# Optimization experiments

Hardware: AMD Instinct MI355X
Metric: run time of the kernel (lower is better)

The kernel has to match this reference:

```python
import jax, jax.numpy as jnp
import numpy as np

MAX_SIZE = 650   # hard-coded node count in the original module
HIDDEN = 512     # hidden_dim
BATCH = 512      # batch_size (conv4 out channels)
IN_DIM = 512
N_EDGES = 150000


def _segment_softmax(e, dst, n):
    # torch_geometric.utils.softmax over destination-node segments
    m = jax.ops.segment_max(e, dst, num_segments=n)
    ex = jnp.exp(e - m[dst])
    s = jax.ops.segment_sum(ex, dst, num_segments=n)
    return ex / (s[dst] + 1e-16)


def _gat_conv(x, src, dst, W, a_src, a_dst, b, n, neg_slope=0.2):
    # PyG GATConv, heads=1, edge_dim=None (edge_attr ignored)
    h = x @ W                            # [n, out]
    al_s = h @ a_src                     # [n] per-node source attention logit
    al_d = h @ a_dst                     # [n] per-node dest attention logit
    e = jax.nn.leaky_relu(al_s[src] + al_d[dst], neg_slope)   # [E]
    alpha = _segment_softmax(e, dst, n)                        # [E]
    out = jax.ops.segment_sum(alpha[:, None] * h[src], dst, num_segments=n)
    return out + b


def setup_inputs() -> dict:
    key = jax.random.key(0)
    ks = jax.random.split(key, 12)
    inp = {
        "x_s": jax.random.normal(ks[0], (400, IN_DIM), jnp.float32),
        "x_t": jax.random.normal(ks[1], (250, IN_DIM), jnp.float32),
        "edge_index": jax.random.randint(ks[2], (2, N_EDGES), 0, MAX_SIZE, dtype=jnp.int32),
        "distances": jax.random.uniform(ks[3], (N_EDGES,), jnp.float32),
        "batch": jnp.zeros((MAX_SIZE,), jnp.int32),
        "W1": jax.random.normal(ks[4], (IN_DIM, HIDDEN), jnp.float32) / np.sqrt(IN_DIM).astype(np.float32),
        "a_src1": jax.random.normal(ks[5], (HIDDEN,), jnp.float32) * 0.1,
        "a_dst1": jax.random.normal(ks[6], (HIDDEN,), jnp.float32) * 0.1,
        "b1": jnp.zeros((HIDDEN,), jnp.float32),
        "W4": jax.random.normal(ks[7], (HIDDEN, BATCH), jnp.float32) / np.sqrt(HIDDEN).astype(np.float32),
        "a_src4": jax.random.normal(ks[8], (BATCH,), jnp.float32) * 0.1,
        "a_dst4": jax.random.normal(ks[9], (BATCH,), jnp.float32) * 0.1,
        "b4": jnp.zeros((BATCH,), jnp.float32),
        "fc_w": jax.random.normal(ks[10], (1, MAX_SIZE), jnp.float32) / np.sqrt(MAX_SIZE).astype(np.float32),
        "fc_b": jnp.zeros((1,), jnp.float32),
    }
    return inp


def reference(x_s, x_t, edge_index, distances, batch,
              W1, a_src1, a_dst1, b1, W4, a_src4, a_dst4, b4, fc_w, fc_b):
    # distances (edge_attr) and batch are unpacked but unused, as in the
    # original (GATConv with edge_dim=None ignores edge_attr).
    x = jnp.concatenate([x_s, x_t], axis=0)
    pad_n = max(MAX_SIZE - x.shape[0], 0)
    x = jnp.pad(x, ((0, pad_n), (0, 0)))            # [650, IN_DIM]
    # add_self_loops=True (PyG GATConv default)
    loop = jnp.arange(MAX_SIZE, dtype=edge_index.dtype)
    src = jnp.concatenate([edge_index[0], loop])
    dst = jnp.concatenate([edge_index[1], loop])
    x = _gat_conv(x, src, dst, W1, a_src1, a_dst1, b1, MAX_SIZE)
    x = jax.nn.relu(x)
    x = _gat_conv(x, src, dst, W4, a_src4, a_dst4, b4, MAX_SIZE)
    x = jax.nn.leaky_relu(x, 0.01)                  # [650, BATCH]
    x = x.reshape(BATCH, MAX_SIZE)                  # torch .view semantics (no transpose)
    x = x @ fc_w.T + fc_b                           # [BATCH, 1]
    x = x.squeeze()[None, :]                        # [1, BATCH]
    return jax.nn.sigmoid(x)
```

## Files before the change

### kernel.cpp

```cpp
#include <hip/hip_runtime.h>
#include <math.h>

#define N_NODES 650
#define DIM     512
#define E_RAW   150000
#define E_TOT   150650

#define BM 16
#define BN 64
#define BK 32
#define KC 128
#define NZ (DIM / KC)
#define CH 1024
#define NB 64

__global__ __launch_bounds__(256)
void gemm_hp(const float* __restrict__ A, const float* __restrict__ Axt,
             const float* __restrict__ B, float* __restrict__ P,
             int M, int a_mode) {
    __shared__ float Ast[BK][BM + 2];
    __shared__ float Bs[BK][BN];
    int t  = threadIdx.x;
    int tx = t & 15, ty = t >> 4;
    int row0 = blockIdx.y * BM, col0 = blockIdx.x * BN;
    int kbase = blockIdx.z * KC;
    float acc[4] = {};

    for (int kb = kbase; kb < kbase + KC; kb += BK) {
        if (t < 128) {
            int m  = t >> 3;
            int kq = (t & 7) * 4;
            int gr = row0 + m;
            float4 v = make_float4(0.f, 0.f, 0.f, 0.f);
            if (gr < M) {
                const float* rowp;
                if (a_mode == 1)
                    rowp = (gr < 400) ? (A + (size_t)gr * DIM) : (Axt + (size_t)(gr - 400) * DIM);
                else
                    rowp = A + (size_t)gr * DIM;
                v = *(const float4*)(rowp + kb + kq);
            }
            Ast[kq + 0][m] = v.x;
            Ast[kq + 1][m] = v.y;
            Ast[kq + 2][m] = v.z;
            Ast[kq + 3][m] = v.w;
        }
        {
            int n4 = (t & 15) * 4;
            int kk = t >> 4;
            #pragma unroll
            for (int p = 0; p < 2; p++)
                *(float4*)&Bs[kk + p * 16][n4] =
                    *(const float4*)&B[(size_t)(kb + kk + p * 16) * DIM + col0 + n4];
        }
        __syncthreads();
        #pragma unroll
        for (int kk = 0; kk < BK; kk++) {
            float a = Ast[kk][ty];
            float4 b4 = *(const float4*)&Bs[kk][tx * 4];
            acc[0] += a * b4.x; acc[1] += a * b4.y;
            acc[2] += a * b4.z; acc[3] += a * b4.w;
        }
        __syncthreads();
    }

    float* Cout = P + (size_t)blockIdx.z * N_NODES * DIM;
    int gr = row0 + ty;
    if (gr < M)
        *(float4*)&Cout[(size_t)gr * DIM + col0 + tx * 4] =
            make_float4(acc[0], acc[1], acc[2], acc[3]);
}

__global__ __launch_bounds__(256)
void reduce_logits(const float* __restrict__ P,
                   const float* __restrict__ asrc, const float* __restrict__ adst,
                   float* __restrict__ h, float* __restrict__ als, float* __restrict__ ald) {
    __shared__ float red[8];
    const size_t S = (size_t)N_NODES * DIM;
    int r = blockIdx.x, t = threadIdx.x;
    size_t base = (size_t)r * DIM;
    float v0 = 0.f, v1 = 0.f;
    #pragma unroll
    for (int z = 0; z < NZ; z++) {
        v0 += P[z * S + base + t];
        v1 += P[z * S + base + t + 256];
    }
    h[base + t]       = v0;
    h[base + t + 256] = v1;
    float ps = v0 * asrc[t] + v1 * asrc[t + 256];
    float pd = v0 * adst[t] + v1 * adst[t + 256];
    #pragma unroll
    for (int o = 32; o > 0; o >>= 1) {
        ps += __shfl_down(ps, o);
        pd += __shfl_down(pd, o);
    }
    if ((t & 63) == 0) { red[t >> 6] = ps; red[4 + (t >> 6)] = pd; }
    __syncthreads();
    if (t == 0) als[r] = red[0] + red[1] + red[2] + red[3];
    if (t == 1) ald[r] = red[4] + red[5] + red[6] + red[7];
}

__global__ __launch_bounds__(256)
void count_kernel(const int* __restrict__ ei, int* __restrict__ cntb) {
    __shared__ int h[N_NODES];
    for (int l = threadIdx.x; l < N_NODES; l += 256) h[l] = 0;
    __syncthreads();
    int per = (E_TOT + NB - 1) / NB;
    int e0 = blockIdx.x * per;
    int e1 = min(e0 + per, E_TOT);
    for (int i = e0 + threadIdx.x; i < e1; i += 256) {
        int d = (i < E_RAW) ? ei[E_RAW + i] : i - E_RAW;
        atomicAdd(&h[d], 1);
    }
    __syncthreads();
    for (int l = threadIdx.x; l < N_NODES; l += 256)
        cntb[blockIdx.x * N_NODES + l] = h[l];
}

__global__ __launch_bounds__(1024)
void scanbase_kernel(const int* __restrict__ cntb, int* __restrict__ rowptr,
                     int* __restrict__ baseb) {
    __shared__ int buf[1024];
    int t = threadIdx.x;
    int tot = 0;
    if (t < N_NODES)
        for (int b = 0; b < NB; b++) tot += cntb[b * N_NODES + t];
    buf[t] = (t < N_NODES) ? tot : 0;
    __syncthreads();
    #pragma unroll
    for (int o = 1; o < 1024; o <<= 1) {
        int v = (t >= o) ? buf[t - o] : 0;
        __syncthreads();
        buf[t] += v;
        __syncthreads();
    }
    if (t < N_NODES) {
        int run = buf[t] - tot;
        rowptr[t] = run;
        for (int b = 0; b < NB; b++) {
            baseb[b * N_NODES + t] = run;
            run += cntb[b * N_NODES + t];
        }
    }
    if (t == 0) rowptr[N_NODES] = E_TOT;
}

__global__ __launch_bounds__(256)
void scatter2_kernel(const int* __restrict__ ei, const int* __restrict__ baseb,
                     int* __restrict__ ssrc) {
    __shared__ int lcur[N_NODES];
    for (int l = threadIdx.x; l < N_NODES; l += 256)
        lcur[l] = baseb[blockIdx.x * N_NODES + l];
    __syncthreads();
    int per = (E_TOT + NB - 1) / NB;
    int e0 = blockIdx.x * per;
    int e1 = min(e0 + per, E_TOT);
    for (int i = e0 + threadIdx.x; i < e1; i += 256) {
        int s, d;
        if (i < E_RAW) { s = ei[i]; d = ei[E_RAW + i]; }
        else           { s = d = i - E_RAW; }
        int pos = atomicAdd(&lcur[d], 1);
        ssrc[pos] = s;
    }
}

__global__ __launch_bounds__(256)
void spmm_kernel(const int* __restrict__ rowptr, const int* __restrict__ ssrc,
                 const float* __restrict__ als, const float* __restrict__ ald,
                 const float* __restrict__ h, const float* __restrict__ bias,
                 float slope, float* __restrict__ outm) {
    __shared__ int   sS[CH];
    __shared__ float sE[CH];
    __shared__ float red[4];
    int d = blockIdx.x;
    int t = threadIdx.x;
    int c = blockIdx.y * 256 + t;
    int r0 = rowptr[d], r1 = rowptr[d + 1];
    int deg = r1 - r0;
    float aldd = ald[d];
    float acc = 0.f, psum = 0.f;

    for (int cb = 0; cb < deg; cb += CH) {
        int n = min(CH, deg - cb);
        __syncthreads();
        for (int l = t; l < n; l += 256) {
            int s = ssrc[r0 + cb + l];
            float v = als[s] + aldd;
            v = v > 0.f ? v : 0.2f * v;
            float ex = __expf(v);
            sS[l] = s;
            sE[l] = ex;
            psum += ex;
        }
        __syncthreads();
        int e = 0;
        for (; e + 4 <= n; e += 4) {
            int   s0 = sS[e],   s1 = sS[e+1], s2 = sS[e+2], s3 = sS[e+3];
            float e0 = sE[e],   e1 = sE[e+1], e2 = sE[e+2], e3 = sE[e+3];
            float x0 = h[(size_t)s0 * DIM + c];
            float x1 = h[(size_t)s1 * DIM + c];
            float x2 = h[(size_t)s2 * DIM + c];
            float x3 = h[(size_t)s3 * DIM + c];
            acc += e0 * x0 + e1 * x1 + e2 * x2 + e3 * x3;
        }
        for (; e < n; e++)
            acc += sE[e] * h[(size_t)sS[e] * DIM + c];
    }

    #pragma unroll
    for (int o = 32; o > 0; o >>= 1) psum += __shfl_down(psum, o);
    if ((t & 63) == 0) red[t >> 6] = psum;
    __syncthreads();
    float sum = red[0] + red[1] + red[2] + red[3];
    float v = acc / (sum + 1e-16f) + bias[c];
    v = v > 0.f ? v : slope * v;
    outm[(size_t)d * DIM + c] = v;
}

__global__ void final_kernel(const float* __restrict__ o2,
                             const float* __restrict__ fcw,
                             const float* __restrict__ fcb,
                             float* __restrict__ out) {
    int b = blockIdx.x * 4 + (threadIdx.x >> 6);
    int lane = threadIdx.x & 63;
    if (b >= 512) return;
    float s = 0.f;
    for (int i = lane; i < N_NODES; i += 64)
        s += o2[b * N_NODES + i] * fcw[i];
    #pragma unroll
    for (int o = 32; o > 0; o >>= 1) s += __shfl_down(s, o);
    if (lane == 0) out[b] = 1.f / (1.f + expf(-(s + fcb[0])));
}

extern "C" void kernel_launch(void* const* d_in, const int* in_sizes, int n_in,
                              void* d_out, int out_size, void* d_ws, size_t ws_size,
                              hipStream_t stream) {
    const float* x_s   = (const float*)d_in[0];
    const float* x_t   = (const float*)d_in[1];
    const int*   ei    = (const int*)d_in[2];
    const float* W1    = (const float*)d_in[5];
    const float* asrc1 = (const float*)d_in[6];
    const float* adst1 = (const float*)d_in[7];
    const float* b1    = (const float*)d_in[8];
    const float* W4    = (const float*)d_in[9];
    const float* asrc4 = (const float*)d_in[10];
    const float* adst4 = (const float*)d_in[11];
    const float* b4    = (const float*)d_in[12];
    const float* fcw   = (const float*)d_in[13];
    const float* fcb   = (const float*)d_in[14];
    float* out = (float*)d_out;

    const size_t H_ELEMS = (size_t)N_NODES * DIM;
    float* ws = (float*)d_ws;
    int*   cntb   = (int*)ws;
    int*   baseb  = cntb + NB * N_NODES;
    int*   rowptr = baseb + NB * N_NODES;
    int*   ssrc   = rowptr + N_NODES + 1;
    float* als1   = (float*)(ssrc + E_TOT);
    float* ald1   = als1 + N_NODES;
    float* als2   = ald1 + N_NODES;
    float* ald2   = als2 + N_NODES;
    float* P      = ald2 + N_NODES;
    float* h1     = P + (size_t)NZ * H_ELEMS;
    float* o1     = h1 + H_ELEMS;
    float* h2     = h1;
    float* o2     = o1;

    dim3 gG(DIM / BN, (N_NODES + BM - 1) / BM, NZ);
    dim3 gS(N_NODES, 2);

    count_kernel<<<NB, 256, 0, stream>>>(ei, cntb);
    scanbase_kernel<<<1, 1024, 0, stream>>>(cntb, rowptr, baseb);
    scatter2_kernel<<<NB, 256, 0, stream>>>(ei, baseb, ssrc);

    gemm_hp<<<gG, 256, 0, stream>>>(x_s, x_t, W1, P, N_NODES, 1);
    reduce_logits<<<N_NODES, 256, 0, stream>>>(P, asrc1, adst1, h1, als1, ald1);
    spmm_kernel<<<gS, 256, 0, stream>>>(rowptr, ssrc, als1, ald1, h1, b1, 0.0f, o1);

    gemm_hp<<<gG, 256, 0, stream>>>(o1, nullptr, W4, P, N_NODES, 0);
    reduce_logits<<<N_NODES, 256, 0, stream>>>(P, asrc4, adst4, h2, als2, ald2);
    spmm_kernel<<<gS, 256, 0, stream>>>(rowptr, ssrc, als2, ald2, h2, b4, 0.01f, o2);

    final_kernel<<<128, 256, 0, stream>>>(o2, fcw, fcb, out);
}
```

Measured before the change: 189.1 us.

## Replace edge-gather SpMM with dense attention matrix GEMM and fuse epilogues

Each destination row's softmax weights are accumulated into a dense 650x650 attention matrix (alpha_build, using shared-memory atomics). Aggregation then runs as a dense GEMM with h, replacing the per-edge gather SpMM over about 150k edges. The GEMM tile grows to 64x64 with a 4x4 register micro-tile and split-K of 2. Bias plus ReLU for layer 1 is fused into the next GEMM's A-load, and bias plus leaky-ReLU for layer 2 into the final kernel. This trades irregular gather traffic for roughly 650^2*512 dense FLOPs per layer and extra workspace.

```diff
diff --git a/kernel.cpp b/kernel.cpp
--- a/kernel.cpp
+++ b/kernel.cpp
@@ -5,70 +5,96 @@
 #define DIM     512
 #define E_RAW   150000
 #define E_TOT   150650
-
-#define BM 16
-#define BN 64
-#define BK 32
-#define KC 128
-#define NZ (DIM / KC)
-#define CH 1024
-#define NB 64
-
-__global__ __launch_bounds__(256)
-void gemm_hp(const float* __restrict__ A, const float* __restrict__ Axt,
-             const float* __restrict__ B, float* __restrict__ P,
-             int M, int a_mode) {
-    __shared__ float Ast[BK][BM + 2];
-    __shared__ float Bs[BK][BN];
+#define NB      64
+#define A_LD    704
+#define S_H     (N_NODES * DIM)
+
+__global__ __launch_bounds__(256)
+void gemm4(const float* __restrict__ A0, const float* __restrict__ A1p,
+           const float* __restrict__ abias, const float* __restrict__ B,
+           float* __restrict__ P, int M, int lda, int Kb, int KC, int a_mode) {
+    __shared__ float Ast[32][68];
+    __shared__ float Bs[32][64];
     int t  = threadIdx.x;
     int tx = t & 15, ty = t >> 4;
-    int row0 = blockIdx.y * BM, col0 = blockIdx.x * BN;
+    int row0 = blockIdx.y * 64, col0 = blockIdx.x * 64;
     int kbase = blockIdx.z * KC;
-    float acc[4] = {};
-
-    for (int kb = kbase; kb < kbase + KC; kb += BK) {
-        if (t < 128) {
-            int m  = t >> 3;
-            int kq = (t & 7) * 4;
-            int gr = row0 + m;
-            float4 v = make_float4(0.f, 0.f, 0.f, 0.f);
-            if (gr < M) {
-                const float* rowp;
-                if (a_mode == 1)
-                    rowp = (gr < 400) ? (A + (size_t)gr * DIM) : (Axt + (size_t)(gr - 400) * DIM);
-                else
-                    rowp = A + (size_t)gr * DIM;
-                v = *(const float4*)(rowp + kb + kq);
+    float acc[4][4] = {};
+    int m   = t >> 2;
+    int kq  = (t & 3) * 4;
+    int bkk = t >> 4;
+    int bn4 = (t & 15) * 4;
+
+    for (int kb = kbase; kb < kbase + KC; kb += 32) {
+        float4 va = make_float4(0.f, 0.f, 0.f, 0.f);
+        float4 vb = make_float4(0.f, 0.f, 0.f, 0.f);
+        int gr = row0 + m;
+        if (gr < M) {
+            if (a_mode == 1) {
+                const float* rp = (gr < 400) ? (A0 + (size_t)gr * 512)
+                                             : (A1p + (size_t)(gr - 400) * 512);
+                va = *(const float4*)(rp + kb + kq);
+                vb = *(const float4*)(rp + kb + kq + 16);
+            } else if (a_mode == 2) {
+                size_t base = (size_t)gr * 512 + kb + kq;
+                float4 p0 = *(const float4*)(A0 + base);
+                float4 p1 = *(const float4*)(A1p + base);
+                float4 bb = *(const float4*)(abias + kb + kq);
+                va.x = p0.x + p1.x + bb.x; va.y = p0.y + p1.y + bb.y;
+                va.z = p0.z + p1.z + bb.z; va.w = p0.w + p1.w + bb.w;
+                p0 = *(const float4*)(A0 + base + 16);
+                p1 = *(const float4*)(A1p + base + 16);
+                bb = *(const float4*)(abias + kb + kq + 16);
+                vb.x = p0.x + p1.x + bb.x; vb.y = p0.y + p1.y + bb.y;
+                vb.z = p0.z + p1.z + bb.z; vb.w = p0.w + p1.w + bb.w;
+                va.x = fmaxf(va.x, 0.f); va.y = fmaxf(va.y, 0.f);
+                va.z = fmaxf(va.z, 0.f); va.w = fmaxf(va.w, 0.f);
+                vb.x = fmaxf(vb.x, 0.f); vb.y = fmaxf(vb.y, 0.f);
+                vb.z = fmaxf(vb.z, 0.f); vb.w = fmaxf(vb.w, 0.f);
+            } else {
+                const float* rp = A0 + (size_t)gr * lda;
+                va = *(const float4*)(rp + kb + kq);
+                vb = *(const float4*)(rp + kb + kq + 16);
             }
-            Ast[kq + 0][m] = v.x;
-            Ast[kq + 1][m] = v.y;
-            Ast[kq + 2][m] = v.z;
-            Ast[kq + 3][m] = v.w;
-        }
+        }
+        Ast[kq + 0][m] = va.x; Ast[kq + 1][m] = va.y;
+        Ast[kq + 2][m] = va.z; Ast[kq + 3][m] = va.w;
+        Ast[kq + 16][m] = vb.x; Ast[kq + 17][m] = vb.y;
+        Ast[kq + 18][m] = vb.z; Ast[kq + 19][m] = vb.w;
         {
-            int n4 = (t & 15) * 4;
-            int kk = t >> 4;
-            #pragma unroll
-            for (int p = 0; p < 2; p++)
-                *(float4*)&Bs[kk + p * 16][n4] =
-                    *(const float4*)&B[(size_t)(kb + kk + p * 16) * DIM + col0 + n4];
+            int gk0 = kb + bkk, gk1 = gk0 + 16;
+            float4 v0 = (gk0 < Kb) ? *(const float4*)&B[(size_t)gk0 * 512 + col0 + bn4]
+                                   : make_float4(0.f, 0.f, 0.f, 0.f);
+            float4 v1 = (gk1 < Kb) ? *(const float4*)&B[(size_t)gk1 * 512 + col0 + bn4]
+                                   : make_float4(0.f, 0.f, 0.f, 0.f);
+            *(float4*)&Bs[bkk][bn4]      = v0;
+            *(float4*)&Bs[bkk + 16][bn4] = v1;
         }
         __syncthreads();
         #pragma unroll
-        for (int kk = 0; kk < BK; kk++) {
-            float a = Ast[kk][ty];
-            float4 b4 = *(const float4*)&Bs[kk][tx * 4];
-            acc[0] += a * b4.x; acc[1] += a * b4.y;
-            acc[2] += a * b4.z; acc[3] += a * b4.w;
-        }
-        __syncthreads();
-    }
-
-    float* Cout = P + (size_t)blockIdx.z * N_NODES * DIM;
-    int gr = row0 + ty;
-    if (gr < M)
-        *(float4*)&Cout[(size_t)gr * DIM + col0 + tx * 4] =
-            make_float4(acc[0], acc[1], acc[2], acc[3]);
+        for (int kk = 0; kk < 32; kk++) {
+            float4 av = *(const float4*)&Ast[kk][ty * 4];
+            float4 bv = *(const float4*)&Bs[kk][tx * 4];
+            acc[0][0] += av.x * bv.x; acc[0][1] += av.x * bv.y;
+            acc[0][2] += av.x * bv.z; acc[0][3] += av.x * bv.w;
+            acc[1][0] += av.y * bv.x; acc[1][1] += av.y * bv.y;
+            acc[1][2] += av.y * bv.z; acc[1][3] += av.y * bv.w;
+            acc[2][0] += av.z * bv.x; acc[2][1] += av.z * bv.y;
+            acc[2][2] += av.z * bv.z; acc[2][3] += av.z * bv.w;
+            acc[3][0] += av.w * bv.x; acc[3][1] += av.w * bv.y;
+            acc[3][2] += av.w * bv.z; acc[3][3] += av.w * bv.w;
+        }
+        __syncthreads();
+    }
+
+    float* Pz = P + (size_t)blockIdx.z * S_H;
+    #pragma unroll
+    for (int i = 0; i < 4; i++) {
+        int gr = row0 + ty * 4 + i;
+        if (gr < M)
+            *(float4*)&Pz[(size_t)gr * 512 + col0 + tx * 4] =
+                make_float4(acc[i][0], acc[i][1], acc[i][2], acc[i][3]);
+    }
 }
 
 __global__ __launch_bounds__(256)
@@ -76,15 +102,10 @@
                    const float* __restrict__ asrc, const float* __restrict__ adst,
                    float* __restrict__ h, float* __restrict__ als, float* __restrict__ ald) {
     __shared__ float red[8];
-    const size_t S = (size_t)N_NODES * DIM;
     int r = blockIdx.x, t = threadIdx.x;
     size_t base = (size_t)r * DIM;
-    float v0 = 0.f, v1 = 0.f;
-    #pragma unroll
-    for (int z = 0; z < NZ; z++) {
-        v0 += P[z * S + base + t];
-        v1 += P[z * S + base + t + 256];
-    }
+    float v0 = P[base + t] + P[S_H + base + t];
+    float v1 = P[base + t + 256] + P[S_H + base + t + 256];
     h[base + t]       = v0;
     h[base + t + 256] = v1;
     float ps = v0 * asrc[t] + v1 * asrc[t + 256];
@@ -165,59 +186,43 @@
 }
 
 __global__ __launch_bounds__(256)
-void spmm_kernel(const int* __restrict__ rowptr, const int* __restrict__ ssrc,
+void alpha_build(const int* __restrict__ rowptr, const int* __restrict__ ssrc,
                  const float* __restrict__ als, const float* __restrict__ ald,
-                 const float* __restrict__ h, const float* __restrict__ bias,
-                 float slope, float* __restrict__ outm) {
-    __shared__ int   sS[CH];
-    __shared__ float sE[CH];
+                 float* __restrict__ Arow) {
+    __shared__ float row[N_NODES];
     __shared__ float red[4];
-    int d = blockIdx.x;
-    int t = threadIdx.x;
-    int c = blockIdx.y * 256 + t;
+    int d = blockIdx.x, t = threadIdx.x;
+    for (int l = t; l < N_NODES; l += 256) row[l] = 0.f;
+    __syncthreads();
     int r0 = rowptr[d], r1 = rowptr[d + 1];
-    int deg = r1 - r0;
     float aldd = ald[d];
-    float acc = 0.f, psum = 0.f;
-
-    for (int cb = 0; cb < deg; cb += CH) {
-        int n = min(CH, deg - cb);
-        __syncthreads();
-        for (int l = t; l < n; l += 256) {
-            int s = ssrc[r0 + cb + l];
-            float v = als[s] + aldd;
-            v = v > 0.f ? v : 0.2f * v;
-            float ex = __expf(v);
-            sS[l] = s;
-            sE[l] = ex;
-            psum += ex;
-        }
-        __syncthreads();
-        int e = 0;
-        for (; e + 4 <= n; e += 4) {
-            int   s0 = sS[e],   s1 = sS[e+1], s2 = sS[e+2], s3 = sS[e+3];
-            float e0 = sE[e],   e1 = sE[e+1], e2 = sE[e+2], e3 = sE[e+3];
-            float x0 = h[(size_t)s0 * DIM + c];
-            float x1 = h[(size_t)s1 * DIM + c];
-            float x2 = h[(size_t)s2 * DIM + c];
-            float x3 = h[(size_t)s3 * DIM + c];
-            acc += e0 * x0 + e1 * x1 + e2 * x2 + e3 * x3;
-        }
-        for (; e < n; e++)
-            acc += sE[e] * h[(size_t)sS[e] * DIM + c];
-    }
-
+    float psum = 0.f;
+    for (int l = r0 + t; l < r1; l += 256) {
+        int s = ssrc[l];
+        float v = als[s] + aldd;
+        v = v > 0.f ? v : 0.2f * v;
+        float ex = __expf(v);
+        atomicAdd(&row[s], ex);
+        psum += ex;
+    }
     #pragma unroll
     for (int o = 32; o > 0; o >>= 1) psum += __shfl_down(psum, o);
     if ((t & 63) == 0) red[t >> 6] = psum;
     __syncthreads();
-    float sum = red[0] + red[1] + red[2] + red[3];
-    float v = acc / (sum + 1e-16f) + bias[c];
-    v = v > 0.f ? v : slope * v;
-    outm[(size_t)d * DIM + c] = v;
-}
-
-__global__ void final_kernel(const float* __restrict__ o2,
+    float inv = 1.f / (red[0] + red[1] + red[2] + red[3] + 1e-16f);
+    for (int q = t; q < A_LD / 4; q += 256) {
+        int c = q * 4;
+        float4 v;
+        v.x = (c + 0 < N_NODES) ? row[c + 0] * inv : 0.f;
+        v.y = (c + 1 < N_NODES) ? row[c + 1] * inv : 0.f;
+        v.z = (c + 2 < N_NODES) ? row[c + 2] * inv : 0.f;
+        v.w = (c + 3 < N_NODES) ? row[c + 3] * inv : 0.f;
+        *(float4*)&Arow[(size_t)d * A_LD + c] = v;
+    }
+}
+
+__global__ void final_kernel(const float* __restrict__ Q,
+                             const float* __restrict__ b4,
                              const float* __restrict__ fcw,
                              const float* __restrict__ fcb,
                              float* __restrict__ out) {
@@ -225,8 +230,12 @@
     int lane = threadIdx.x & 63;
     if (b >= 512) return;
     float s = 0.f;
-    for (int i = lane; i < N_NODES; i += 64)
-        s += o2[b * N_NODES + i] * fcw[i];
+    for (int i = lane; i < N_NODES; i += 64) {
+        int g = b * N_NODES + i;
+        float v = Q[g] + Q[S_H + g] + b4[g & 511];
+        v = v > 0.f ? v : 0.01f * v;
+        s += v * fcw[i];
+    }
     #pragma unroll
     for (int o = 32; o > 0; o >>= 1) s += __shfl_down(s, o);
     if (lane == 0) out[b] = 1.f / (1.f + expf(-(s + fcb[0])));
@@ -250,7 +259,6 @@
     const float* fcb   = (const float*)d_in[14];
     float* out = (float*)d_out;
 
-    const size_t H_ELEMS = (size_t)N_NODES * DIM;
     float* ws = (float*)d_ws;
     int*   cntb   = (int*)ws;
     int*   baseb  = cntb + NB * N_NODES;
@@ -260,26 +268,28 @@
     float* ald1   = als1 + N_NODES;
     float* als2   = ald1 + N_NODES;
     float* ald2   = als2 + N_NODES;
-    float* P      = ald2 + N_NODES;
-    float* h1     = P + (size_t)NZ * H_ELEMS;
-    float* o1     = h1 + H_ELEMS;
-    float* h2     = h1;
-    float* o2     = o1;
-
-    dim3 gG(DIM / BN, (N_NODES + BM - 1) / BM, NZ);
-    dim3 gS(N_NODES, 2);
+    float* A1     = ald2 + N_NODES;
+    float* A2     = A1 + (size_t)N_NODES * A_LD;
+    float* P      = A2 + (size_t)N_NODES * A_LD;
+    float* Q      = P + 2 * (size_t)S_H;
+    float* h1     = Q + 2 * (size_t)S_H;
+    float* h2     = h1 + (size_t)S_H;
+
+    dim3 gG(8, 11, 2);
 
     count_kernel<<<NB, 256, 0, stream>>>(ei, cntb);
     scanbase_kernel<<<1, 1024, 0, stream>>>(cntb, rowptr, baseb);
     scatter2_kernel<<<NB, 256, 0, stream>>>(ei, baseb, ssrc);
 
-    gemm_hp<<<gG, 256, 0, stream>>>(x_s, x_t, W1, P, N_NODES, 1);
+    gemm4<<<gG, 256, 0, stream>>>(x_s, x_t, nullptr, W1, P, N_NODES, 512, 512, 256, 1);
     reduce_logits<<<N_NODES, 256, 0, stream>>>(P, asrc1, adst1, h1, als1, ald1);
-    spmm_kernel<<<gS, 256, 0, stream>>>(rowptr, ssrc, als1, ald1, h1, b1, 0.0f, o1);
-
-    gemm_hp<<<gG, 256, 0, stream>>>(o1, nullptr, W4, P, N_NODES, 0);
+    alpha_build<<<N_NODES, 256, 0, stream>>>(rowptr, ssrc, als1, ald1, A1);
+    gemm4<<<gG, 256, 0, stream>>>(A1, nullptr, nullptr, h1, Q, N_NODES, A_LD, N_NODES, 352, 0);
+
+    gemm4<<<gG, 256, 0, stream>>>(Q, Q + S_H, b1, W4, P, N_NODES, 512, 512, 256, 2);
     reduce_logits<<<N_NODES, 256, 0, stream>>>(P, asrc4, adst4, h2, als2, ald2);
-    spmm_kernel<<<gS, 256, 0, stream>>>(rowptr, ssrc, als2, ald2, h2, b4, 0.01f, o2);
-
-    final_kernel<<<128, 256, 0, stream>>>(o2, fcw, fcb, out);
-}
+    alpha_build<<<N_NODES, 256, 0, stream>>>(rowptr, ssrc, als2, ald2, A2);
+    gemm4<<<gG, 256, 0, stream>>>(A2, nullptr, nullptr, h2, Q, N_NODES, A_LD, N_NODES, 352, 0);
+
+    final_kernel<<<128, 256, 0, stream>>>(Q, b4, fcw, fcb, out);
+}
```

New measurement: 201.2 us. 6.4% more time.
